# Optimization experiments

Hardware: AMD Instinct MI355X
Metric: run time of the kernel (lower is better)

## Reference

```python
import jax, jax.numpy as jnp
import numpy as np

# Model dims (match init_kwargs)
D_MODEL = 512
N_LAYERS = 4
N_DIST = 32
N_CAT = 32
LATENT = N_DIST * N_CAT  # 1024
D_INNER = 2 * D_MODEL    # 1024 (mamba expand=2)
D_STATE = 16
DT_RANK = D_MODEL // 16  # 32
K = 4                    # depthwise conv kernel
BATCH, SEQ = 4, 1024


def setup_inputs() -> dict:
    key = jax.random.key(0)
    ks = jax.random.split(key, 12)
    f = lambda k, shape, s=0.02: (jax.random.normal(k, shape, jnp.float32) * s)
    inp = {
        "x": jax.random.normal(ks[0], (BATCH, SEQ, LATENT), jnp.float32),
        "lin1_w": f(ks[1], (LATENT, D_MODEL)),
        "lin1_b": jnp.zeros((D_MODEL,), jnp.float32),
        "norm_w": jnp.ones((N_LAYERS, D_MODEL), jnp.float32),
        "in_w": f(ks[2], (N_LAYERS, D_MODEL, 2 * D_INNER)),
        "conv_w": f(ks[3], (N_LAYERS, D_INNER, K), 0.1),
        "conv_b": jnp.zeros((N_LAYERS, D_INNER), jnp.float32),
        "xproj_w": f(ks[4], (N_LAYERS, D_INNER, DT_RANK + 2 * D_STATE)),
        "dt_w": f(ks[5], (N_LAYERS, DT_RANK, D_INNER)),
        "dt_b": f(ks[6], (N_LAYERS, D_INNER), 0.5),
        "A_log": jnp.log(jnp.broadcast_to(
            jnp.arange(1, D_STATE + 1, dtype=jnp.float32),
            (N_LAYERS, D_INNER, D_STATE))),
        "Dp": jnp.ones((N_LAYERS, D_INNER), jnp.float32),
        "out_w": f(ks[7], (N_LAYERS, D_INNER, D_MODEL)),
        "lin2_w": f(ks[8], (D_MODEL, LATENT)),
        "lin2_b": jnp.zeros((LATENT,), jnp.float32),
    }
    return inp


def _rmsnorm(x, w):
    return x * jax.lax.rsqrt(jnp.mean(x * x, axis=-1, keepdims=True) + 1e-5) * w


def _causal_dwconv(x, w, b):
    # x: (B,S,D), w: (D,K) -> depthwise causal conv1d, left-padded
    S = x.shape[1]
    xp = jnp.pad(x, ((0, 0), (K - 1, 0), (0, 0)))
    y = xp[:, 0:S, :] * w[:, 0]
    for k in range(1, K):
        y = y + xp[:, k:k + S, :] * w[:, k]
    return y + b


def _selective_scan(u, dt, Bm, Cm, A, Dvec):
    # u, dt: (B,S,D); Bm, Cm: (B,S,N); A: (D,N); Dvec: (D,)
    dA = jnp.exp(dt[..., None] * A)                               # (B,S,D,N)
    dBu = dt[..., None] * Bm[:, :, None, :] * u[..., None]        # (B,S,D,N)
    h0 = jnp.zeros((u.shape[0], u.shape[2], A.shape[1]), u.dtype)

    def step(h, inputs):
        dA_t, dBu_t, C_t = inputs
        h = dA_t * h + dBu_t                                       # (B,D,N)
        y = jnp.einsum('bdn,bn->bd', h, C_t)
        return h, y

    _, ys = jax.lax.scan(step, h0,
                         (dA.transpose(1, 0, 2, 3),
                          dBu.transpose(1, 0, 2, 3),
                          Cm.transpose(1, 0, 2)))
    return ys.transpose(1, 0, 2) + u * Dvec                       # (B,S,D)


def reference(x, lin1_w, lin1_b, norm_w, in_w, conv_w, conv_b, xproj_w,
              dt_w, dt_b, A_log, Dp, out_w, lin2_w, lin2_b):
    B, S, _ = x.shape
    h = x @ lin1_w + lin1_b                                       # (B,S,d_model)
    for l in range(N_LAYERS):
        resid = h
        hn = _rmsnorm(h, norm_w[l])
        xz = hn @ in_w[l]                                         # (B,S,2*d_inner)
        xp, z = jnp.split(xz, 2, axis=-1)
        xp = jax.nn.silu(_causal_dwconv(xp, conv_w[l], conv_b[l]))
        dbl = xp @ xproj_w[l]                                     # (B,S,dt_rank+2N)
        dt = jax.nn.softplus(dbl[..., :DT_RANK] @ dt_w[l] + dt_b[l])
        Bm = dbl[..., DT_RANK:DT_RANK + D_STATE]
        Cm = dbl[..., DT_RANK + D_STATE:]
        A = -jnp.exp(A_log[l])                                    # (d_inner, N)
        y = _selective_scan(xp, dt, Bm, Cm, A, Dp[l])
        y = y * jax.nn.silu(z)
        h = resid + y @ out_w[l]
    out = h @ lin2_w + lin2_b                                     # (B,S,latent)
    out = jax.nn.softmax(out.reshape(B, S, N_DIST, N_CAT), axis=-1)
    return out.reshape(B, S, N_DIST * N_CAT)
```

## Files before the change

kernel.cpp:

```cpp
#include <hip/hip_runtime.h>
#include <math.h>

#define D_MODEL 512
#define N_LAYERS 4
#define LATENT 1024
#define D_INNER 1024
#define D_STATE 16
#define DT_RANK 32
#define KCONV 4
#define BATCH 4
#define SEQ 1024
#define NTOK (BATCH * SEQ)
#define PCH 32
#define CLEN 32
#define NCAT 1152

typedef __attribute__((ext_vector_type(8))) short short8;
typedef __attribute__((ext_vector_type(4))) float floatx4;
typedef unsigned short ushort_t;

#define WC_VM4   0x0F74
#define WC_VM0   0x0F70
#define WC_LGKM0 0xC07F

__device__ __forceinline__ ushort_t f2bf(float f) {
    union { float f; unsigned u; } v; v.f = f;
    unsigned r = v.u + 0x7FFFu + ((v.u >> 16) & 1u);
    return (ushort_t)(r >> 16);
}
__device__ __forceinline__ float bf2f(ushort_t u) {
    union { unsigned u; float f; } v; v.u = ((unsigned)u) << 16;
    return v.f;
}
__device__ __forceinline__ void gll16(const void* g, void* l) {
    __builtin_amdgcn_global_load_lds(
        (const __attribute__((address_space(1))) void*)g,
        (__attribute__((address_space(3))) void*)l, 16, 0, 0);
}

__global__ __launch_bounds__(256, 4) void gemm_bf16_kernel(
    const ushort_t* __restrict__ A, int lda,
    const ushort_t* __restrict__ Bt, int ldb,
    float* __restrict__ C, ushort_t* __restrict__ Cb, int ldc,
    const float* __restrict__ bias,
    int M, int N, int K, int flags)
{
    __shared__ ushort_t As[2][4096];
    __shared__ ushort_t Bs[2][4096];
    const int tid = threadIdx.x;
    const int m0 = blockIdx.y * 64;
    const int n0 = blockIdx.x * 64;
    const int w = tid >> 6;
    const int lane = tid & 63;
    const int quad = lane >> 4;
    const int l16 = lane & 15;
    const int wm = (w & 1) * 32;
    const int wn = (w >> 1) * 32;

    const ushort_t* ga = A + (size_t)(m0 + (tid >> 2)) * lda + (tid & 3) * 8;
    const ushort_t* gb = Bt + (size_t)(n0 + (tid >> 2)) * ldb + (tid & 3) * 8;
    const int lofs = tid * 8;

    floatx4 acc[2][2] = {};
    const int nt = K >> 6;

    gll16(ga, &As[0][lofs]);
    gll16(ga + 32, &As[0][2048 + lofs]);
    gll16(gb, &Bs[0][lofs]);
    gll16(gb + 32, &Bs[0][2048 + lofs]);

    for (int kt = 0; kt < nt; kt++) {
        const int cur = kt & 1;
        if (kt + 1 < nt) {
            const ushort_t* pa = ga + (kt + 1) * 64;
            const ushort_t* pb = gb + (kt + 1) * 64;
            gll16(pa, &As[1 - cur][lofs]);
            gll16(pa + 32, &As[1 - cur][2048 + lofs]);
            gll16(pb, &Bs[1 - cur][lofs]);
            gll16(pb + 32, &Bs[1 - cur][2048 + lofs]);
            __builtin_amdgcn_s_waitcnt(WC_VM4);
        } else {
            __builtin_amdgcn_s_waitcnt(WC_VM0);
        }
        __builtin_amdgcn_s_barrier();

        short8 af[2][2], bfr[2][2];
        #pragma unroll
        for (int ks = 0; ks < 2; ks++) {
            #pragma unroll
            for (int i = 0; i < 2; i++)
                af[ks][i] = *(const short8*)&As[cur][ks * 2048 + (wm + i * 16 + l16) * 32 + quad * 8];
            #pragma unroll
            for (int j = 0; j < 2; j++)
                bfr[ks][j] = *(const short8*)&Bs[cur][ks * 2048 + (wn + j * 16 + l16) * 32 + quad * 8];
        }
        __builtin_amdgcn_s_waitcnt(WC_LGKM0);
        __builtin_amdgcn_s_barrier();

        #pragma unroll
        for (int ks = 0; ks < 2; ks++)
            #pragma unroll
            for (int i = 0; i < 2; i++)
                #pragma unroll
                for (int j = 0; j < 2; j++)
                    acc[i][j] = __builtin_amdgcn_mfma_f32_16x16x32_bf16(
                        af[ks][i], bfr[ks][j], acc[i][j], 0, 0, 0);
    }

    #pragma unroll
    for (int j = 0; j < 2; j++) {
        int n = n0 + wn + j * 16 + l16;
        float bv = (flags & 1) ? bias[n] : 0.f;
        bool do_sp = (flags & 4) && (n < 1024);
        float spb = do_sp ? bias[n] : 0.f;
        #pragma unroll
        for (int i = 0; i < 2; i++) {
            int mrow = m0 + wm + i * 16 + quad * 4;
            #pragma unroll
            for (int rr = 0; rr < 4; rr++) {
                size_t idx = (size_t)(mrow + rr) * ldc + n;
                float v = acc[i][j][rr] + bv;
                if (do_sp) {
                    v += spb;
                    v = (v > 20.f) ? v : log1pf(__expf(v));
                }
                if (flags & 8) {
                    Cb[idx] = f2bf(v);
                } else {
                    if (flags & 2) v += C[idx];
                    C[idx] = v;
                }
            }
        }
    }
}

__global__ __launch_bounds__(256) void build_wdt_kernel(
    const float* __restrict__ xproj_w, const float* __restrict__ dt_w,
    ushort_t* __restrict__ wcat)
{
    const int l = blockIdx.z;
    const int n0 = blockIdx.x * 64;
    const int k0 = blockIdx.y * 64;
    const float* xw  = xproj_w + (size_t)l * D_INNER * 64;
    const float* dtw = dt_w + (size_t)l * DT_RANK * D_INNER;

    __shared__ float xs[64][33];
    __shared__ float ds[32][65];

    const int tid = threadIdx.x;
    {
        int row = tid >> 2;
        int col = (tid & 3) * 8;
        #pragma unroll
        for (int q = 0; q < 8; q++)
            xs[row][col + q] = xw[(size_t)(k0 + row) * 64 + col + q];
    }
    {
        int row = tid >> 3;
        int col = (tid & 7) * 8;
        #pragma unroll
        for (int q = 0; q < 8; q++)
            ds[row][col + q] = dtw[(size_t)row * D_INNER + n0 + col + q];
    }
    __syncthreads();

    const int ty = tid & 15;
    const int tx = tid >> 4;
    float acc[4][4] = {};
    #pragma unroll
    for (int r = 0; r < 32; r++) {
        float a[4], b[4];
        #pragma unroll
        for (int i = 0; i < 4; i++) a[i] = xs[ty * 4 + i][r];
        #pragma unroll
        for (int j = 0; j < 4; j++) b[j] = ds[r][tx * 4 + j];
        #pragma unroll
        for (int j = 0; j < 4; j++)
            #pragma unroll
            for (int i = 0; i < 4; i++)
                acc[j][i] = fmaf(a[i], b[j], acc[j][i]);
    }
    #pragma unroll
    for (int j = 0; j < 4; j++) {
        int n = n0 + tx * 4 + j;
        ushort4 o;
        o.x = f2bf(acc[j][0]); o.y = f2bf(acc[j][1]);
        o.z = f2bf(acc[j][2]); o.w = f2bf(acc[j][3]);
        *(ushort4*)&wcat[((size_t)l * NCAT + n) * D_INNER + k0 + ty * 4] = o;
    }
}

__global__ __launch_bounds__(256) void build_wbc_kernel(
    const float* __restrict__ xproj_w, ushort_t* __restrict__ wcat)
{
    const int idx = blockIdx.x * 256 + threadIdx.x;
    const int k = idx & 1023;
    const int j = (idx >> 10) & 127;
    const int l = idx >> 17;
    ushort_t v = 0;
    if (j < 32)
        v = f2bf(xproj_w[((size_t)l * D_INNER + k) * 64 + 32 + j]);
    wcat[((size_t)l * NCAT + 1024 + j) * D_INNER + k] = v;
}

__global__ __launch_bounds__(256) void transpose_cast_kernel(
    const float* __restrict__ in, ushort_t* __restrict__ out, int K, int N)
{
    __shared__ float tile[32][33];
    const int n0 = blockIdx.x * 32, k0 = blockIdx.y * 32;
    const int tx = threadIdx.x & 31, ty = threadIdx.x >> 5;
    #pragma unroll
    for (int i = 0; i < 4; i++)
        tile[ty + i * 8][tx] = in[(size_t)(k0 + ty + i * 8) * N + n0 + tx];
    __syncthreads();
    #pragma unroll
    for (int i = 0; i < 4; i++)
        out[(size_t)(n0 + ty + i * 8) * K + k0 + tx] = f2bf(tile[tx][ty + i * 8]);
}

__global__ __launch_bounds__(256) void cast_bf16_kernel(
    const float* __restrict__ in, ushort_t* __restrict__ out)
{
    const int i = blockIdx.x * 256 + threadIdx.x;
    out[i] = f2bf(in[i]);
}

__global__ __launch_bounds__(256) void rmsnorm_kernel(
    const float* __restrict__ x, const float* __restrict__ w,
    ushort_t* __restrict__ y)
{
    const int row = blockIdx.x;
    const float* xr = x + (size_t)row * D_MODEL;
    ushort_t* yr = y + (size_t)row * D_MODEL;
    const int tid = threadIdx.x;

    float v0 = xr[tid], v1 = xr[tid + 256];
    float ss = v0 * v0 + v1 * v1;
    #pragma unroll
    for (int off = 32; off > 0; off >>= 1) ss += __shfl_down(ss, off);

    __shared__ float wsum[4];
    __shared__ float scale_s;
    int wid = tid >> 6, lane = tid & 63;
    if (lane == 0) wsum[wid] = ss;
    __syncthreads();
    if (tid == 0) {
        float tot = wsum[0] + wsum[1] + wsum[2] + wsum[3];
        scale_s = 1.0f / sqrtf(tot / (float)D_MODEL + 1e-5f);
    }
    __syncthreads();
    float sc = scale_s;
    yr[tid] = f2bf(v0 * sc * w[tid]);
    yr[tid + 256] = f2bf(v1 * sc * w[tid + 256]);
}

__global__ __launch_bounds__(256) void conv_silu_kernel(
    const ushort_t* __restrict__ xz, const float* __restrict__ w,
    const float* __restrict__ bconv, ushort_t* __restrict__ outb)
{
    const int idx = blockIdx.x * 256 + threadIdx.x;
    const int d = idx & (D_INNER - 1);
    const int t = (idx >> 10) & (SEQ - 1);
    const int row = idx >> 10;
    const ushort_t* base = xz + (size_t)row * 2048 + d;

    float s = 0.f;
    #pragma unroll
    for (int k = 0; k < KCONV; k++) {
        int tt = t + k - (KCONV - 1);
        if (tt >= 0)
            s = fmaf(bf2f(base[(ptrdiff_t)(k - (KCONV - 1)) * 2048]), w[d * KCONV + k], s);
    }
    s += bconv[d];
    float r = s / (1.f + __expf(-s));
    outb[idx] = f2bf(r);
}

__global__ __launch_bounds__(256) void scan_pass1(
    const float* __restrict__ dbl, const ushort_t* __restrict__ ub,
    const float* __restrict__ A_log,
    float* __restrict__ hfin, float* __restrict__ sumdt)
{
    const int tid = threadIdx.x;
    const int b = blockIdx.x >> 7;
    const int p = (blockIdx.x >> 2) & 31;
    const int d = ((blockIdx.x & 3) << 8) + tid;
    const int t0 = p * CLEN;

    float A[D_STATE];
    #pragma unroll
    for (int n = 0; n < D_STATE; n++) A[n] = -expf(A_log[d * D_STATE + n]);

    float h[D_STATE] = {};
    float sdt = 0.f;

    const float* dtp = dbl + ((size_t)b * SEQ + t0) * NCAT + d;
    const float* bp  = dbl + ((size_t)b * SEQ + t0) * NCAT + 1024;
    const ushort_t* up = ub + ((size_t)b * SEQ + t0) * D_INNER + d;

    for (int t = 0; t < CLEN; t++) {
        float dtv = dtp[(size_t)t * NCAT];
        float uv  = bf2f(up[(size_t)t * D_INNER]);
        float dtu = dtv * uv;
        sdt += dtv;
        #pragma unroll
        for (int n = 0; n < D_STATE; n++)
            h[n] = fmaf(__expf(dtv * A[n]), h[n], dtu * bp[t * NCAT + n]);
    }

    size_t base = (size_t)(b * PCH + p) * D_STATE * D_INNER + d;
    #pragma unroll
    for (int n = 0; n < D_STATE; n++) hfin[base + (size_t)n * D_INNER] = h[n];
    sumdt[(size_t)(b * PCH + p) * D_INNER + d] = sdt;
}

__global__ __launch_bounds__(256) void scan_pass2(
    const float* __restrict__ A_log, const float* __restrict__ sumdt,
    float* __restrict__ hc)
{
    const int tid = threadIdx.x;
    const int b = blockIdx.x >> 6;
    const int n = (blockIdx.x >> 2) & 15;
    const int d = ((blockIdx.x & 3) << 8) + tid;

    const float Aval = -expf(A_log[d * D_STATE + n]);
    float h = 0.f;
    for (int p = 0; p < PCH; p++) {
        size_t idx = ((size_t)(b * PCH + p) * D_STATE + n) * D_INNER + d;
        float fin = hc[idx];
        hc[idx] = h;
        h = fmaf(__expf(Aval * sumdt[(size_t)(b * PCH + p) * D_INNER + d]), h, fin);
    }
}

__global__ __launch_bounds__(256) void scan_pass3(
    const float* __restrict__ dbl, const ushort_t* __restrict__ xz,
    const float* __restrict__ A_log, const float* __restrict__ Dp,
    const float* __restrict__ hstart, ushort_t* ub)
{
    const int tid = threadIdx.x;
    const int b = blockIdx.x >> 7;
    const int p = (blockIdx.x >> 2) & 31;
    const int d = ((blockIdx.x & 3) << 8) + tid;
    const int t0 = p * CLEN;

    float A[D_STATE];
    #pragma unroll
    for (int n = 0; n < D_STATE; n++) A[n] = -expf(A_log[d * D_STATE + n]);
    const float Dv = Dp[d];

    float h[D_STATE];
    size_t base = (size_t)(b * PCH + p) * D_STATE * D_INNER + d;
    #pragma unroll
    for (int n = 0; n < D_STATE; n++) h[n] = hstart[base + (size_t)n * D_INNER];

    const float* dtp = dbl + ((size_t)b * SEQ + t0) * NCAT + d;
    const float* bp  = dbl + ((size_t)b * SEQ + t0) * NCAT + 1024;
    const ushort_t* zp = xz + ((size_t)b * SEQ + t0) * 2048 + 1024 + d;
    ushort_t* up = ub + ((size_t)b * SEQ + t0) * D_INNER + d;

    for (int t = 0; t < CLEN; t++) {
        float dtv = dtp[(size_t)t * NCAT];
        float uv  = bf2f(up[(size_t)t * D_INNER]);
        float zv  = bf2f(zp[(size_t)t * 2048]);
        float dtu = dtv * uv;
        float y = 0.f;
        #pragma unroll
        for (int n = 0; n < D_STATE; n++) {
            h[n] = fmaf(__expf(dtv * A[n]), h[n], dtu * bp[t * NCAT + n]);
            y = fmaf(h[n], bp[t * NCAT + 16 + n], y);
        }
        float res = fmaf(uv, Dv, y);
        res *= zv / (1.f + __expf(-zv));
        up[(size_t)t * D_INNER] = f2bf(res);
    }
}

__global__ __launch_bounds__(256) void softmax_kernel(
    const float* __restrict__ in, float* __restrict__ out)
{
    const int idx = blockIdx.x * 256 + threadIdx.x;
    float v = in[idx];
    float m = v;
    #pragma unroll
    for (int off = 16; off > 0; off >>= 1) m = fmaxf(m, __shfl_xor(m, off, 32));
    float e = expf(v - m);
    float s = e;
    #pragma unroll
    for (int off = 16; off > 0; off >>= 1) s += __shfl_xor(s, off, 32);
    out[idx] = e / s;
}

extern "C" void kernel_launch(void* const* d_in, const int* in_sizes, int n_in,
                              void* d_out, int out_size, void* d_ws, size_t ws_size,
                              hipStream_t stream)
{
    const float* x       = (const float*)d_in[0];
    const float* lin1_w  = (const float*)d_in[1];
    const float* lin1_b  = (const float*)d_in[2];
    const float* norm_w  = (const float*)d_in[3];
    const float* in_w    = (const float*)d_in[4];
    const float* conv_w  = (const float*)d_in[5];
    const float* conv_b  = (const float*)d_in[6];
    const float* xproj_w = (const float*)d_in[7];
    const float* dt_w    = (const float*)d_in[8];
    const float* dt_b    = (const float*)d_in[9];
    const float* A_log   = (const float*)d_in[10];
    const float* Dp      = (const float*)d_in[11];
    const float* out_w   = (const float*)d_in[12];
    const float* lin2_w  = (const float*)d_in[13];
    const float* lin2_b  = (const float*)d_in[14];
    float* outp = (float*)d_out;
    (void)ws_size; (void)in_sizes; (void)n_in; (void)out_size;

    float* ws = (float*)d_ws;
    const size_t F1M = 1u << 20;
    float* h     = ws;
    float* dbl   = h + 2 * F1M;
    float* sumdt = dbl + (size_t)NTOK * NCAT;
    float* hfin  = sumdt + (size_t)BATCH * PCH * D_INNER;
    ushort_t* xzb   = (ushort_t*)(hfin + 2 * F1M);
    ushort_t* hn_bf = xzb + 8 * F1M;
    ushort_t* xb    = hn_bf + 2 * F1M;
    ushort_t* lin1_wt = xb + 4 * F1M;
    ushort_t* in_wt   = lin1_wt + (size_t)512 * 1024;
    ushort_t* out_wt  = in_wt + (size_t)4 * 2048 * 512;
    ushort_t* lin2_wt = out_wt + (size_t)4 * 512 * 1024;
    ushort_t* wcat    = lin2_wt + (size_t)1024 * 512;

    dim3 blk(256);

    transpose_cast_kernel<<<dim3(512 / 32, 1024 / 32), blk, 0, stream>>>(
        lin1_w, lin1_wt, LATENT, D_MODEL);
    for (int l = 0; l < N_LAYERS; l++) {
        transpose_cast_kernel<<<dim3(2048 / 32, 512 / 32), blk, 0, stream>>>(
            in_w + (size_t)l * 512 * 2048, in_wt + (size_t)l * 2048 * 512, 512, 2048);
        transpose_cast_kernel<<<dim3(512 / 32, 1024 / 32), blk, 0, stream>>>(
            out_w + (size_t)l * 1024 * 512, out_wt + (size_t)l * 512 * 1024, 1024, 512);
    }
    transpose_cast_kernel<<<dim3(1024 / 32, 512 / 32), blk, 0, stream>>>(
        lin2_w, lin2_wt, D_MODEL, LATENT);
    build_wdt_kernel<<<dim3(16, 16, N_LAYERS), blk, 0, stream>>>(
        xproj_w, dt_w, wcat);
    build_wbc_kernel<<<dim3((N_LAYERS * 128 * 1024) / 256), blk, 0, stream>>>(
        xproj_w, wcat);

    cast_bf16_kernel<<<dim3((NTOK * LATENT) / 256), blk, 0, stream>>>(x, xb);

    gemm_bf16_kernel<<<dim3(D_MODEL / 64, NTOK / 64), blk, 0, stream>>>(
        xb, LATENT, lin1_wt, LATENT, h, nullptr, D_MODEL, lin1_b,
        NTOK, D_MODEL, LATENT, 1);

    for (int l = 0; l < N_LAYERS; l++) {
        const float* nw = norm_w + (size_t)l * D_MODEL;
        const float* cw = conv_w + (size_t)l * D_INNER * KCONV;
        const float* cb = conv_b + (size_t)l * D_INNER;
        const float* db = dt_b + (size_t)l * D_INNER;
        const float* al = A_log + (size_t)l * D_INNER * D_STATE;
        const float* dp = Dp + (size_t)l * D_INNER;
        const ushort_t* iwt = in_wt + (size_t)l * 2048 * 512;
        const ushort_t* owt = out_wt + (size_t)l * 512 * 1024;
        const ushort_t* wc  = wcat + (size_t)l * NCAT * D_INNER;

        rmsnorm_kernel<<<dim3(NTOK), blk, 0, stream>>>(h, nw, hn_bf);

        gemm_bf16_kernel<<<dim3(2048 / 64, NTOK / 64), blk, 0, stream>>>(
            hn_bf, D_MODEL, iwt, D_MODEL, nullptr, xzb, 2048, nullptr,
            NTOK, 2048, D_MODEL, 8);

        conv_silu_kernel<<<dim3((NTOK * D_INNER) / 256), blk, 0, stream>>>(
            xzb, cw, cb, xb);

        gemm_bf16_kernel<<<dim3(NCAT / 64, NTOK / 64), blk, 0, stream>>>(
            xb, D_INNER, wc, D_INNER, dbl, nullptr, NCAT, db,
            NTOK, NCAT, D_INNER, 4);

        scan_pass1<<<dim3(BATCH * PCH * (D_INNER / 256)), blk, 0, stream>>>(
            dbl, xb, al, hfin, sumdt);
        scan_pass2<<<dim3(BATCH * D_STATE * (D_INNER / 256)), blk, 0, stream>>>(
            al, sumdt, hfin);
        scan_pass3<<<dim3(BATCH * PCH * (D_INNER / 256)), blk, 0, stream>>>(
            dbl, xzb, al, dp, hfin, xb);

        gemm_bf16_kernel<<<dim3(D_MODEL / 64, NTOK / 64), blk, 0, stream>>>(
            xb, D_INNER, owt, D_INNER, h, nullptr, D_MODEL, nullptr,
            NTOK, D_MODEL, D_INNER, 2);
    }

    cast_bf16_kernel<<<dim3((NTOK * D_MODEL) / 256), blk, 0, stream>>>(h, xb);
    gemm_bf16_kernel<<<dim3(LATENT / 64, NTOK / 64), blk, 0, stream>>>(
        xb, D_MODEL, lin2_wt, D_MODEL, dbl, nullptr, LATENT, lin2_b,
        NTOK, LATENT, D_MODEL, 1);
    softmax_kernel<<<dim3((NTOK * LATENT) / 256), blk, 0, stream>>>(dbl, outp);
}
```

Baseline: 779.6 us.

## Enlarge GEMM tiles to 128xBN with XOR-swizzled LDS layout

Replaces the 64x64 bf16 MFMA GEMM with a templated kernel using 128-row tiles and either 64 or 128 columns. Each wave now computes a 64xBN/2 sub-tile, and each K step covers the full 64-wide slice. The shared-memory layout uses an XOR swizzle on 16-byte chunks to avoid bank conflicts. The larger tiles raise arithmetic intensity and data reuse, at the cost of more registers and LDS per block, lower occupancy, and fewer blocks for small GEMMs.

New measurement: 837.5 us. +7.4%, slower.

```diff
diff --git a/kernel.cpp b/kernel.cpp
--- a/kernel.cpp
+++ b/kernel.cpp
@@ -19,7 +19,6 @@
 typedef __attribute__((ext_vector_type(4))) float floatx4;
 typedef unsigned short ushort_t;
 
-#define WC_VM4   0x0F74
 #define WC_VM0   0x0F70
 #define WC_LGKM0 0xC07F
 
@@ -38,61 +37,82 @@
         (__attribute__((address_space(3))) void*)l, 16, 0, 0);
 }
 
-__global__ __launch_bounds__(256, 4) void gemm_bf16_kernel(
+template<int BN>
+__global__ __launch_bounds__(256, (BN == 64) ? 3 : 2) void gemm_bf16_tile(
     const ushort_t* __restrict__ A, int lda,
     const ushort_t* __restrict__ Bt, int ldb,
     float* __restrict__ C, ushort_t* __restrict__ Cb, int ldc,
     const float* __restrict__ bias,
     int M, int N, int K, int flags)
 {
-    __shared__ ushort_t As[2][4096];
-    __shared__ ushort_t Bs[2][4096];
+    constexpr int BM = 128;
+    constexpr int NJ = BN / 32;
+    constexpr int AOPS = 4;
+    constexpr int BOPS = BN / 32;
+    constexpr int NOPS = AOPS + BOPS;
+    constexpr int WC_PREF = 0x0F70 | NOPS;
+
+    __shared__ ushort_t As[2][BM * 64];
+    __shared__ ushort_t Bs[2][BN * 64];
+
     const int tid = threadIdx.x;
-    const int m0 = blockIdx.y * 64;
-    const int n0 = blockIdx.x * 64;
+    const int m0 = blockIdx.y * BM;
+    const int n0 = blockIdx.x * BN;
     const int w = tid >> 6;
     const int lane = tid & 63;
     const int quad = lane >> 4;
     const int l16 = lane & 15;
-    const int wm = (w & 1) * 32;
-    const int wn = (w >> 1) * 32;
-
-    const ushort_t* ga = A + (size_t)(m0 + (tid >> 2)) * lda + (tid & 3) * 8;
-    const ushort_t* gb = Bt + (size_t)(n0 + (tid >> 2)) * ldb + (tid & 3) * 8;
+    const int wm = (w & 1) * 64;
+    const int wn = (w >> 1) * (BN / 2);
+
+    const int srow = tid >> 3;
+    const int schunk = ((tid & 7) ^ (srow & 7)) * 8;
+    const ushort_t* ga = A + (size_t)(m0 + srow) * lda + schunk;
+    const ushort_t* gb = Bt + (size_t)(n0 + srow) * ldb + schunk;
     const int lofs = tid * 8;
 
-    floatx4 acc[2][2] = {};
+    const int swz0 = ((0 * 4 + quad) ^ (l16 & 7)) * 8;
+    const int swz1 = ((1 * 4 + quad) ^ (l16 & 7)) * 8;
+
+    floatx4 acc[4][NJ] = {};
     const int nt = K >> 6;
 
-    gll16(ga, &As[0][lofs]);
-    gll16(ga + 32, &As[0][2048 + lofs]);
-    gll16(gb, &Bs[0][lofs]);
-    gll16(gb + 32, &Bs[0][2048 + lofs]);
+    #pragma unroll
+    for (int q = 0; q < AOPS; q++)
+        gll16(ga + (size_t)q * 32 * lda, &As[0][q * 2048 + lofs]);
+    #pragma unroll
+    for (int q = 0; q < BOPS; q++)
+        gll16(gb + (size_t)q * 32 * ldb, &Bs[0][q * 2048 + lofs]);
 
     for (int kt = 0; kt < nt; kt++) {
         const int cur = kt & 1;
         if (kt + 1 < nt) {
             const ushort_t* pa = ga + (kt + 1) * 64;
             const ushort_t* pb = gb + (kt + 1) * 64;
-            gll16(pa, &As[1 - cur][lofs]);
-            gll16(pa + 32, &As[1 - cur][2048 + lofs]);
-            gll16(pb, &Bs[1 - cur][lofs]);
-            gll16(pb + 32, &Bs[1 - cur][2048 + lofs]);
-            __builtin_amdgcn_s_waitcnt(WC_VM4);
+            #pragma unroll
+            for (int q = 0; q < AOPS; q++)
+                gll16(pa + (size_t)q * 32 * lda, &As[1 - cur][q * 2048 + lofs]);
+            #pragma unroll
+            for (int q = 0; q < BOPS; q++)
+                gll16(pb + (size_t)q * 32 * ldb, &Bs[1 - cur][q * 2048 + lofs]);
+            __builtin_amdgcn_s_waitcnt(WC_PREF);
         } else {
             __builtin_amdgcn_s_waitcnt(WC_VM0);
         }
         __builtin_amdgcn_s_barrier();
 
-        short8 af[2][2], bfr[2][2];
-        #pragma unroll
-        for (int ks = 0; ks < 2; ks++) {
-            #pragma unroll
-            for (int i = 0; i < 2; i++)
-                af[ks][i] = *(const short8*)&As[cur][ks * 2048 + (wm + i * 16 + l16) * 32 + quad * 8];
-            #pragma unroll
-            for (int j = 0; j < 2; j++)
-                bfr[ks][j] = *(const short8*)&Bs[cur][ks * 2048 + (wn + j * 16 + l16) * 32 + quad * 8];
+        short8 af[2][4], bfr[2][NJ];
+        #pragma unroll
+        for (int i = 0; i < 4; i++) {
+            const int r = wm + i * 16 + l16;
+            af[0][i] = *(const short8*)&As[cur][r * 64 + swz0];
+            af[1][i] = *(const short8*)&As[cur][r * 64 + swz1];
+        }
+        #pragma unroll
+        for (int j = 0; j < NJ; j++) {
+            const int r = wn + j * 16 + l16;
+            bfr[0][j] = *(const short8*)&Bs[cur][r * 64 + swz0];
+            bfr[1][j] = *(const short8*)&Bs[cur][r * 64 + swz1];
         }
         __builtin_amdgcn_s_waitcnt(WC_LGKM0);
         __builtin_amdgcn_s_barrier();
@@ -100,21 +120,21 @@
         #pragma unroll
         for (int ks = 0; ks < 2; ks++)
             #pragma unroll
-            for (int i = 0; i < 2; i++)
+            for (int i = 0; i < 4; i++)
                 #pragma unroll
-                for (int j = 0; j < 2; j++)
+                for (int j = 0; j < NJ; j++)
                     acc[i][j] = __builtin_amdgcn_mfma_f32_16x16x32_bf16(
                         af[ks][i], bfr[ks][j], acc[i][j], 0, 0, 0);
     }
 
     #pragma unroll
-    for (int j = 0; j < 2; j++) {
+    for (int j = 0; j < NJ; j++) {
         int n = n0 + wn + j * 16 + l16;
         float bv = (flags & 1) ? bias[n] : 0.f;
         bool do_sp = (flags & 4) && (n < 1024);
         float spb = do_sp ? bias[n] : 0.f;
         #pragma unroll
-        for (int i = 0; i < 2; i++) {
+        for (int i = 0; i < 4; i++) {
             int mrow = m0 + wm + i * 16 + quad * 4;
             #pragma unroll
             for (int rr = 0; rr < 4; rr++) {
@@ -448,7 +468,7 @@
 
     cast_bf16_kernel<<<dim3((NTOK * LATENT) / 256), blk, 0, stream>>>(x, xb);
 
-    gemm_bf16_kernel<<<dim3(D_MODEL / 64, NTOK / 64), blk, 0, stream>>>(
+    gemm_bf16_tile<64><<<dim3(D_MODEL / 64, NTOK / 128), blk, 0, stream>>>(
         xb, LATENT, lin1_wt, LATENT, h, nullptr, D_MODEL, lin1_b,
         NTOK, D_MODEL, LATENT, 1);
 
@@ -465,14 +485,14 @@
 
         rmsnorm_kernel<<<dim3(NTOK), blk, 0, stream>>>(h, nw, hn_bf);
 
-        gemm_bf16_kernel<<<dim3(2048 / 64, NTOK / 64), blk, 0, stream>>>(
+        gemm_bf16_tile<128><<<dim3(2048 / 128, NTOK / 128), blk, 0, stream>>>(
             hn_bf, D_MODEL, iwt, D_MODEL, nullptr, xzb, 2048, nullptr,
             NTOK, 2048, D_MODEL, 8);
 
         conv_silu_kernel<<<dim3((NTOK * D_INNER) / 256), blk, 0, stream>>>(
             xzb, cw, cb, xb);
 
-        gemm_bf16_kernel<<<dim3(NCAT / 64, NTOK / 64), blk, 0, stream>>>(
+        gemm_bf16_tile<64><<<dim3(NCAT / 64, NTOK / 128), blk, 0, stream>>>(
             xb, D_INNER, wc, D_INNER, dbl, nullptr, NCAT, db,
             NTOK, NCAT, D_INNER, 4);
 
@@ -483,13 +503,13 @@
         scan_pass3<<<dim3(BATCH * PCH * (D_INNER / 256)), blk, 0, stream>>>(
             dbl, xzb, al, dp, hfin, xb);
 
-        gemm_bf16_kernel<<<dim3(D_MODEL / 64, NTOK / 64), blk, 0, stream>>>(
+        gemm_bf16_tile<64><<<dim3(D_MODEL / 64, NTOK / 128), blk, 0, stream>>>(
             xb, D_INNER, owt, D_INNER, h, nullptr, D_MODEL, nullptr,
             NTOK, D_MODEL, D_INNER, 2);
     }
 
     cast_bf16_kernel<<<dim3((NTOK * D_MODEL) / 256), blk, 0, stream>>>(h, xb);
-    gemm_bf16_kernel<<<dim3(LATENT / 64, NTOK / 64), blk, 0, stream>>>(
+    gemm_bf16_tile<64><<<dim3(LATENT / 64, NTOK / 128), blk, 0, stream>>>(
         xb, D_MODEL, lin2_wt, D_MODEL, dbl, nullptr, LATENT, lin2_b,
         NTOK, LATENT, D_MODEL, 1);
     softmax_kernel<<<dim3((NTOK * LATENT) / 256), blk, 0, stream>>>(dbl, outp);
```

## Triple-buffer GEMM LDS pipeline with XOR swizzle and XCD-aware block remap

Applied to the files above, without the earlier changes.

Reworks the bf16 MFMA GEMM. The shared-memory pipeline goes from two to three stages, issuing loads two k-tiles ahead and removing the second barrier per iteration. The LDS layout changes to 64-element rows with an XOR-swizzled chunk index, which is meant to avoid bank conflicts on fragment reads. Workgroup IDs are also remapped so that adjacent tiles land on the same XCD for better L2 reuse. The cost is more LDS per block (48KB) and a lower occupancy hint of 3.

Result: no change. 782.8 us (+0.4%).

```diff
diff --git a/kernel.cpp b/kernel.cpp
--- a/kernel.cpp
+++ b/kernel.cpp
@@ -38,18 +38,26 @@
         (__attribute__((address_space(3))) void*)l, 16, 0, 0);
 }
 
-__global__ __launch_bounds__(256, 4) void gemm_bf16_kernel(
+__global__ __launch_bounds__(256, 3) void gemm_bf16_tile(
     const ushort_t* __restrict__ A, int lda,
     const ushort_t* __restrict__ Bt, int ldb,
     float* __restrict__ C, ushort_t* __restrict__ Cb, int ldc,
     const float* __restrict__ bias,
     int M, int N, int K, int flags)
 {
-    __shared__ ushort_t As[2][4096];
-    __shared__ ushort_t Bs[2][4096];
+    __shared__ ushort_t As[3][4096];
+    __shared__ ushort_t Bs[3][4096];
+
+    const int gx = gridDim.x;
+    const int nwg = gx * gridDim.y;
+    const int orig = blockIdx.y * gx + blockIdx.x;
+    const int qq = nwg >> 3, rr = nwg & 7;
+    const int xcd = orig & 7, loc = orig >> 3;
+    const int swz = (xcd < rr ? xcd * (qq + 1) : rr * (qq + 1) + (xcd - rr) * qq) + loc;
+    const int m0 = (swz / gx) * 64;
+    const int n0 = (swz % gx) * 64;
+
     const int tid = threadIdx.x;
-    const int m0 = blockIdx.y * 64;
-    const int n0 = blockIdx.x * 64;
     const int w = tid >> 6;
     const int lane = tid & 63;
     const int quad = lane >> 4;
@@ -57,45 +65,58 @@
     const int wm = (w & 1) * 32;
     const int wn = (w >> 1) * 32;
 
-    const ushort_t* ga = A + (size_t)(m0 + (tid >> 2)) * lda + (tid & 3) * 8;
-    const ushort_t* gb = Bt + (size_t)(n0 + (tid >> 2)) * ldb + (tid & 3) * 8;
+    const int srow = tid >> 3;
+    const int schunk = ((tid & 7) ^ (srow & 7)) * 8;
+    const ushort_t* ga = A + (size_t)(m0 + srow) * lda + schunk;
+    const ushort_t* gb = Bt + (size_t)(n0 + srow) * ldb + schunk;
     const int lofs = tid * 8;
+
+    const int swz0 = ((0 * 4 + quad) ^ (l16 & 7)) * 8;
+    const int swz1 = ((1 * 4 + quad) ^ (l16 & 7)) * 8;
 
     floatx4 acc[2][2] = {};
     const int nt = K >> 6;
 
-    gll16(ga, &As[0][lofs]);
-    gll16(ga + 32, &As[0][2048 + lofs]);
-    gll16(gb, &Bs[0][lofs]);
-    gll16(gb + 32, &Bs[0][2048 + lofs]);
-
+    #define STAGE(t, b)                                         \
+        do {                                                    \
+            const ushort_t* pa_ = ga + (t) * 64;                \
+            const ushort_t* pb_ = gb + (t) * 64;                \
+            gll16(pa_, &As[(b)][lofs]);                         \
+            gll16(pa_ + (size_t)32 * lda, &As[(b)][2048 + lofs]); \
+            gll16(pb_, &Bs[(b)][lofs]);                         \
+            gll16(pb_ + (size_t)32 * ldb, &Bs[(b)][2048 + lofs]); \
+        } while (0)
+
+    STAGE(0, 0);
+    if (nt > 1) STAGE(1, 1);
+
+    int cur = 0;
     for (int kt = 0; kt < nt; kt++) {
-        const int cur = kt & 1;
-        if (kt + 1 < nt) {
-            const ushort_t* pa = ga + (kt + 1) * 64;
-            const ushort_t* pb = gb + (kt + 1) * 64;
-            gll16(pa, &As[1 - cur][lofs]);
-            gll16(pa + 32, &As[1 - cur][2048 + lofs]);
-            gll16(pb, &Bs[1 - cur][lofs]);
-            gll16(pb + 32, &Bs[1 - cur][2048 + lofs]);
-            __builtin_amdgcn_s_waitcnt(WC_VM4);
-        } else {
-            __builtin_amdgcn_s_waitcnt(WC_VM0);
+        if (kt + 1 < nt) __builtin_amdgcn_s_waitcnt(WC_VM4);
+        else             __builtin_amdgcn_s_waitcnt(WC_VM0);
+        __builtin_amdgcn_s_barrier();
+        __builtin_amdgcn_sched_barrier(0);
+
+        if (kt + 2 < nt) {
+            int nb = cur + 2; if (nb >= 3) nb -= 3;
+            STAGE(kt + 2, nb);
         }
-        __builtin_amdgcn_s_barrier();
 
         short8 af[2][2], bfr[2][2];
         #pragma unroll
-        for (int ks = 0; ks < 2; ks++) {
-            #pragma unroll
-            for (int i = 0; i < 2; i++)
-                af[ks][i] = *(const short8*)&As[cur][ks * 2048 + (wm + i * 16 + l16) * 32 + quad * 8];
-            #pragma unroll
-            for (int j = 0; j < 2; j++)
-                bfr[ks][j] = *(const short8*)&Bs[cur][ks * 2048 + (wn + j * 16 + l16) * 32 + quad * 8];
+        for (int i = 0; i < 2; i++) {
+            const int r = wm + i * 16 + l16;
+            af[0][i] = *(const short8*)&As[cur][r * 64 + swz0];
+            af[1][i] = *(const short8*)&As[cur][r * 64 + swz1];
+        }
+        #pragma unroll
+        for (int j = 0; j < 2; j++) {
+            const int r = wn + j * 16 + l16;
+            bfr[0][j] = *(const short8*)&Bs[cur][r * 64 + swz0];
+            bfr[1][j] = *(const short8*)&Bs[cur][r * 64 + swz1];
         }
         __builtin_amdgcn_s_waitcnt(WC_LGKM0);
-        __builtin_amdgcn_s_barrier();
+        __builtin_amdgcn_sched_barrier(0);
 
         #pragma unroll
         for (int ks = 0; ks < 2; ks++)
@@ -105,7 +126,10 @@
                 for (int j = 0; j < 2; j++)
                     acc[i][j] = __builtin_amdgcn_mfma_f32_16x16x32_bf16(
                         af[ks][i], bfr[ks][j], acc[i][j], 0, 0, 0);
-    }
+
+        cur++; if (cur == 3) cur = 0;
+    }
+    #undef STAGE
 
     #pragma unroll
     for (int j = 0; j < 2; j++) {
@@ -117,9 +141,9 @@
         for (int i = 0; i < 2; i++) {
             int mrow = m0 + wm + i * 16 + quad * 4;
             #pragma unroll
-            for (int rr = 0; rr < 4; rr++) {
-                size_t idx = (size_t)(mrow + rr) * ldc + n;
-                float v = acc[i][j][rr] + bv;
+            for (int rr2 = 0; rr2 < 4; rr2++) {
+                size_t idx = (size_t)(mrow + rr2) * ldc + n;
+                float v = acc[i][j][rr2] + bv;
                 if (do_sp) {
                     v += spb;
                     v = (v > 20.f) ? v : log1pf(__expf(v));
@@ -448,7 +472,7 @@
 
     cast_bf16_kernel<<<dim3((NTOK * LATENT) / 256), blk, 0, stream>>>(x, xb);
 
-    gemm_bf16_kernel<<<dim3(D_MODEL / 64, NTOK / 64), blk, 0, stream>>>(
+    gemm_bf16_tile<<<dim3(D_MODEL / 64, NTOK / 64), blk, 0, stream>>>(
         xb, LATENT, lin1_wt, LATENT, h, nullptr, D_MODEL, lin1_b,
         NTOK, D_MODEL, LATENT, 1);
 
@@ -465,14 +489,14 @@
 
         rmsnorm_kernel<<<dim3(NTOK), blk, 0, stream>>>(h, nw, hn_bf);
 
-        gemm_bf16_kernel<<<dim3(2048 / 64, NTOK / 64), blk, 0, stream>>>(
+        gemm_bf16_tile<<<dim3(2048 / 64, NTOK / 64), blk, 0, stream>>>(
             hn_bf, D_MODEL, iwt, D_MODEL, nullptr, xzb, 2048, nullptr,
             NTOK, 2048, D_MODEL, 8);
 
         conv_silu_kernel<<<dim3((NTOK * D_INNER) / 256), blk, 0, stream>>>(
             xzb, cw, cb, xb);
 
-        gemm_bf16_kernel<<<dim3(NCAT / 64, NTOK / 64), blk, 0, stream>>>(
+        gemm_bf16_tile<<<dim3(NCAT / 64, NTOK / 64), blk, 0, stream>>>(
             xb, D_INNER, wc, D_INNER, dbl, nullptr, NCAT, db,
             NTOK, NCAT, D_INNER, 4);
 
@@ -483,13 +507,13 @@
         scan_pass3<<<dim3(BATCH * PCH * (D_INNER / 256)), blk, 0, stream>>>(
             dbl, xzb, al, dp, hfin, xb);
 
-        gemm_bf16_kernel<<<dim3(D_MODEL / 64, NTOK / 64), blk, 0, stream>>>(
+        gemm_bf16_tile<<<dim3(D_MODEL / 64, NTOK / 64), blk, 0, stream>>>(
             xb, D_INNER, owt, D_INNER, h, nullptr, D_MODEL, nullptr,
             NTOK, D_MODEL, D_INNER, 2);
     }
 
     cast_bf16_kernel<<<dim3((NTOK * D_MODEL) / 256), blk, 0, stream>>>(h, xb);
-    gemm_bf16_kernel<<<dim3(LATENT / 64, NTOK / 64), blk, 0, stream>>>(
+    gemm_bf16_tile<<<dim3(LATENT / 64, NTOK / 64), blk, 0, stream>>>(
         xb, D_MODEL, lin2_wt, D_MODEL, dbl, nullptr, LATENT, lin2_b,
         NTOK, LATENT, D_MODEL, 1);
     softmax_kernel<<<dim3((NTOK * LATENT) / 256), blk, 0, stream>>>(dbl, outp);
```
